# Performance work log

Measured on AMD Instinct MI355X. Metric: run time of the kernel, lower is better.

## Reference

```python
import jax, jax.numpy as jnp
import numpy as np

BN_EPS = 1e-5

def setup_inputs() -> dict:
    key = jax.random.key(0)
    ks = jax.random.split(key, 13)
    bs, ch, hei, wei = 4, 32, 32, 128  # n_features = wei = 128, ch = n_features//4
    nf = wei
    def p(k, shape, s=0.05):
        return jax.random.normal(k, shape, dtype=jnp.float32) * s
    return {
        "head": jax.random.normal(ks[0], (bs, ch, hei, wei), dtype=jnp.float32),
        "tail": jax.random.normal(ks[1], (bs, ch, hei, wei), dtype=jnp.float32),
        "R_q": p(ks[2], (nf, nf)), "R_k": p(ks[3], (nf, nf)),
        "R_v": p(ks[4], (nf, nf)), "R_W": p(ks[5], (nf, nf)),
        "F_q": p(ks[6], (nf, nf)), "F_k": p(ks[7], (nf, nf)),
        "F_v": p(ks[8], (nf, nf)), "F_W": p(ks[9], (nf, nf)),
        "conv_w": p(ks[10], (2, 2 * ch, 1, 1)),
        "conv_b": jnp.zeros((2,), jnp.float32),
        "bn_w": jnp.ones((2,), jnp.float32),
        "bn_b": jnp.zeros((2,), jnp.float32),
        "bn_mean": jnp.zeros((2,), jnp.float32),
        "bn_var": jnp.ones((2,), jnp.float32),
        "flag": 1,
    }

def _affinity(head, tail, conv_w, conv_b, bn_w, bn_b, bn_mean, bn_var):
    # 1x1 conv -> eval-mode BatchNorm2d -> ReLU -> softmax over channel dim
    x = jnp.concatenate([head, tail], axis=1)                       # [b,2c,h,w]
    a = jnp.einsum('bchw,oc->bohw', x, conv_w[:, :, 0, 0]) + conv_b[None, :, None, None]
    scale = (bn_w / jnp.sqrt(bn_var + BN_EPS))[None, :, None, None]
    a = (a - bn_mean[None, :, None, None]) * scale + bn_b[None, :, None, None]
    a = jax.nn.relu(a)
    return jax.nn.softmax(a, axis=1)                                # torch legacy dim=1 for 4D

def reference(head, tail, R_q, R_k, R_v, R_W, F_q, F_k, F_v, F_W,
              conv_w, conv_b, bn_w, bn_b, bn_mean, bn_var, flag):
    bs, ch, hei, wei = head.shape
    L = hei * wei
    ic = ch  # inter_channels == ch by construction
    aff = _affinity(head, tail, conv_w, conv_b, bn_w, bn_b, bn_mean, bn_var)
    if flag:
        alpha = aff[:, 0].reshape(bs, L, 1)                          # broadcast over last axis
        q = (head @ R_q).reshape(bs, ic, L).transpose(0, 2, 1)       # [b,L,ic]
        t_k = (tail @ F_k).reshape(bs, ic, L).transpose(0, 2, 1)     # [b,L,ic]
        t_v = (tail @ F_v).reshape(bs, ic, L)                        # [b,ic,L]
        f_t = t_k @ t_v                                              # [b,L,L]
        h_k = (head @ R_k).reshape(bs, ic, L).transpose(0, 2, 1)
        h_v = (head @ R_v).reshape(bs, ic, L)
        f_h = h_k @ h_v                                              # [b,L,L]
        att = jax.nn.softmax(alpha * f_t + f_h, axis=-1)
        y = (att @ q).transpose(0, 2, 1).reshape(bs, ic, hei, wei)
        return y @ R_W + head
    else:
        alpha = aff[:, 1].reshape(bs, L, 1)
        q = (tail @ F_q).reshape(bs, ic, L).transpose(0, 2, 1)
        h_k = (head @ R_k).reshape(bs, ic, L).transpose(0, 2, 1)
        h_v = (head @ R_v).reshape(bs, ic, L)
        f_h = h_k @ h_v
        t_k = (tail @ F_k).reshape(bs, ic, L).transpose(0, 2, 1)
        t_v = (tail @ F_v).reshape(bs, ic, L)
        f_t = t_k @ t_v
        att = jax.nn.softmax(alpha * f_h + f_t, axis=-1)
        y = (att @ q).transpose(0, 2, 1).reshape(bs, ic, hei, wei)
        return y @ F_W + tail
```

## Files before the change

### kernel.cpp

```cpp
#include <hip/hip_runtime.h>
#include <hip/hip_bf16.h>
#include <stdint.h>

typedef unsigned short u16;
typedef unsigned int u32;
typedef __attribute__((ext_vector_type(8))) short short8;
typedef __attribute__((ext_vector_type(4))) short short4_t;
typedef __attribute__((ext_vector_type(4))) float f32x4;

#define MFMA16(A,B,C) __builtin_amdgcn_mfma_f32_16x16x32_bf16((A),(B),(C),0,0,0)
#define L2E 1.4426950408889634f

__device__ __forceinline__ u16 f2bf(float f) {
  u32 x = __float_as_uint(f);
  u32 r = x + 0x7fffu + ((x >> 16) & 1u);
  return (u16)(r >> 16);
}
__device__ __forceinline__ float bf2f(short v) {
  return __uint_as_float((u32)(u16)v << 16);
}
__device__ __forceinline__ u32 pack_bf2(float a, float b) {
  __hip_bfloat162 h = __float22bfloat162_rn(make_float2(a, b));
  u32 u; __builtin_memcpy(&u, &h, 4); return u;
}
__device__ __forceinline__ short8 mk_frag(u32 w0, u32 w1, u32 w2, u32 w3) {
  union { u32 u[4]; short8 s; } cv;
  cv.u[0] = w0; cv.u[1] = w1; cv.u[2] = w2; cv.u[3] = w3;
  return cv.s;
}

__global__ void kprep(const float* R_q, const float* R_k, const float* R_v,
                      const float* R_W, const float* F_q, const float* F_k,
                      const float* F_v, const float* F_W, const int* flagp,
                      u16* matT)
{
  int flag = *flagp;
  const float* S;
  int m = blockIdx.x;
  if (flag) {
    const float* s[6] = {R_q, R_k, R_v, F_k, F_v, R_W}; S = s[m];
  } else {
    const float* s[6] = {F_q, F_k, F_v, R_k, R_v, F_W}; S = s[m];
  }
  u16* dst = matT + m * 16384;
  int base = blockIdx.y * 2048;
  for (int idx = base + threadIdx.x; idx < base + 2048; idx += blockDim.x) {
    int k = idx >> 7, n = idx & 127;
    dst[n * 128 + k] = f2bf(S[idx]);
  }
}

__global__ __launch_bounds__(256) void kproj(const float* __restrict__ head,
    const float* __restrict__ tail, const u16* __restrict__ matT,
    const float* __restrict__ conv_w, const float* __restrict__ conv_b,
    const float* __restrict__ bn_w, const float* __restrict__ bn_b,
    const float* __restrict__ bn_mean, const float* __restrict__ bn_var,
    u16* __restrict__ qT, u16* __restrict__ KQ,
    u16* __restrict__ Vc, const int* __restrict__ flagp)
{
  __shared__ u16 lds_t[128][34];
  __shared__ float s_alpha[128];
  const int flag = *flagp;
  const float* X1 = flag ? head : tail;
  const float* X2 = flag ? tail : head;
  const int bh = blockIdx.x, g = blockIdx.y;
  const int b = bh >> 5, h = bh & 31;
  const float* src = (g < 3) ? X1 : X2;
  const u16* Bm = matT + g * 16384;
  const int tid = threadIdx.x, lane = tid & 63, wid = tid >> 6;
  const int lrow = lane & 15, lg = lane >> 4;
  const int rt = wid & 1, cbase = (wid >> 1) * 64;

  if (g == 3) {
    if (tid < 128) {
      int w = tid;
      const float* hp = head + ((size_t)b * 1024 + h) * 128 + w;
      const float* tp = tail + ((size_t)b * 1024 + h) * 128 + w;
      float a0 = 0.f, a1 = 0.f;
      for (int c = 0; c < 32; ++c) {
        float xh = hp[c * 4096];
        float xt = tp[c * 4096];
        a0 += xh * conv_w[c]      + xt * conv_w[32 + c];
        a1 += xh * conv_w[64 + c] + xt * conv_w[96 + c];
      }
      const float eps = 1e-5f;
      a0 += conv_b[0]; a1 += conv_b[1];
      a0 = (a0 - bn_mean[0]) * (bn_w[0] * rsqrtf(bn_var[0] + eps)) + bn_b[0];
      a1 = (a1 - bn_mean[1]) * (bn_w[1] * rsqrtf(bn_var[1] + eps)) + bn_b[1];
      a0 = fmaxf(a0, 0.f); a1 = fmaxf(a1, 0.f);
      float asel = flag ? a0 : a1, aoth = flag ? a1 : a0;
      s_alpha[w] = 1.f / (1.f + __expf(aoth - asel));
    }
    __syncthreads();
  }

  f32x4 acc[4] = {};
  const float* Arow = src + (((size_t)b * 32 + rt * 16 + lrow) * 32 + h) * 128;
  #pragma unroll
  for (int k0 = 0; k0 < 128; k0 += 32) {
    short8 af;
    const float* ap = Arow + k0 + lg * 8;
    #pragma unroll
    for (int j = 0; j < 8; ++j) af[j] = (short)f2bf(ap[j]);
    #pragma unroll
    for (int cc = 0; cc < 4; ++cc) {
      short8 bf = *reinterpret_cast<const short8*>(
          Bm + (cbase + cc * 16 + lrow) * 128 + k0 + lg * 8);
      acc[cc] = MFMA16(af, bf, acc[cc]);
    }
  }
  #pragma unroll
  for (int cc = 0; cc < 4; ++cc) {
    int n = cbase + cc * 16 + lrow;
    float asc = (g == 1) ? L2E : 1.f;
    if (g == 3) asc = s_alpha[n] * L2E;
    #pragma unroll
    for (int rr = 0; rr < 4; ++rr) {
      int c = rt * 16 + lg * 4 + rr;
      lds_t[n][c] = f2bf(acc[cc][rr] * asc);
    }
  }
  __syncthreads();
  if (g == 0) {
    int c = tid >> 3, w0 = (tid & 7) * 16;
    int tw[8];
    #pragma unroll
    for (int i2 = 0; i2 < 8; ++i2)
      tw[i2] = (int)lds_t[w0 + 2 * i2][c] | ((int)lds_t[w0 + 2 * i2 + 1][c] << 16);
    int4* dst = reinterpret_cast<int4*>(qT + ((size_t)b * 32 + c) * 4096 + h * 128 + w0);
    dst[0] = make_int4(tw[0], tw[1], tw[2], tw[3]);
    dst[1] = make_int4(tw[4], tw[5], tw[6], tw[7]);
  } else if (tid < 128) {
    int w = tid;
    int tw[16];
    #pragma unroll
    for (int i2 = 0; i2 < 16; ++i2)
      tw[i2] = (int)lds_t[w][2 * i2] | ((int)lds_t[w][2 * i2 + 1] << 16);
    u16* base = (g == 2 || g == 4) ? Vc : KQ;
    int coff = (g >= 3) ? 32 : 0;
    int4* dst = reinterpret_cast<int4*>(base + ((size_t)b * 4096 + h * 128 + w) * 64 + coff);
    dst[0] = make_int4(tw[0],  tw[1],  tw[2],  tw[3]);
    dst[1] = make_int4(tw[4],  tw[5],  tw[6],  tw[7]);
    dst[2] = make_int4(tw[8],  tw[9],  tw[10], tw[11]);
    dst[3] = make_int4(tw[12], tw[13], tw[14], tw[15]);
  }
}

__global__ __launch_bounds__(256, 6) void kattn(const u16* __restrict__ qT,
    const u16* __restrict__ KQ, const u16* __restrict__ Vc,
    u16* __restrict__ pO, float* __restrict__ pm, float* __restrict__ pl)
{
  __shared__ __align__(16) char lds_v[2][8192];
  __shared__ __align__(16) char lds_q[2][4096];
  const int b = blockIdx.y;
  const int i0 = blockIdx.x * 64;
  const int sp = blockIdx.z;
  const int jbase = sp * 512;
  const int tid = threadIdx.x, lane = tid & 63, wid = tid >> 6;
  const int lrow = lane & 15, lg = lane >> 4;

  const u16* KQb = KQ + (size_t)b * 4096 * 64;
  const u16* Vb  = Vc + (size_t)b * 4096 * 64;
  const u16* qTb = qT + (size_t)b * 32 * 4096;

  short8 bkq[2];
  {
    int r = i0 + wid * 16 + lrow;
    #pragma unroll
    for (int kc = 0; kc < 2; ++kc)
      bkq[kc] = *reinterpret_cast<const short8*>(KQb + (size_t)r * 64 + kc * 32 + lg * 8);
  }

  const int sr = tid >> 3, sx = (tid & 7) * 16;
  const int pr = (((sr >> 2) & 3) << 3) + (((sr >> 4) & 1) << 2) + (sr & 3);

  #pragma unroll
  for (int q = 0; q < 2; ++q) {
    int r = sr + q * 32, gr = pr + q * 32;
    int4 v = *reinterpret_cast<const int4*>(
        reinterpret_cast<const char*>(Vb + (size_t)(jbase + gr) * 64) + sx);
    *reinterpret_cast<int4*>(lds_v[0] + r * 128 + (sx ^ ((r & 7) << 4))) = v;
  }
  {
    int4 qv = *reinterpret_cast<const int4*>(
        qTb + (size_t)sr * 4096 + jbase + (tid & 7) * 8);
    *reinterpret_cast<int4*>(lds_q[0] + sr * 128 + (sx ^ ((sr & 7) << 4))) = qv;
  }
  __syncthreads();

  float m_run = -1e30f, l_run = 0.f;
  f32x4 accO[2] = {};
  int4 stgV[2], stgQ;

  for (int t = 0; t < 8; ++t) {
    const int buf = t & 1;
    if (t < 7) {
      const u16* Vn = Vb + (size_t)(jbase + (t + 1) * 64) * 64;
      #pragma unroll
      for (int q = 0; q < 2; ++q) {
        int gr = pr + q * 32;
        stgV[q] = *reinterpret_cast<const int4*>(
            reinterpret_cast<const char*>(Vn + (size_t)gr * 64) + sx);
      }
      stgQ = *reinterpret_cast<const int4*>(
          qTb + (size_t)sr * 4096 + jbase + (t + 1) * 64 + (tid & 7) * 8);
    }
    f32x4 st[4];
    __builtin_amdgcn_s_setprio(1);
    #pragma unroll
    for (int sub = 0; sub < 4; ++sub) {
      f32x4 a = {};
      #pragma unroll
      for (int kc = 0; kc < 2; ++kc) {
        int r = sub * 16 + lrow;
        int xs = kc * 64 + lg * 16;
        short8 av = *reinterpret_cast<const short8*>(
            lds_v[buf] + r * 128 + (xs ^ ((r & 7) << 4)));
        a = MFMA16(av, bkq[kc], a);
      }
      st[sub] = a;
    }
    __builtin_amdgcn_s_setprio(0);
    short8 aq[2][2];
    #pragma unroll
    for (int w = 0; w < 2; ++w)
      #pragma unroll
      for (int ct = 0; ct < 2; ++ct) {
        int r = ct * 16 + lrow;
        int xs = w * 64 + lg * 16;
        aq[w][ct] = *reinterpret_cast<const short8*>(
            lds_q[buf] + r * 128 + (xs ^ ((r & 7) << 4)));
      }
    float tm = -1e30f;
    #pragma unroll
    for (int sub = 0; sub < 4; ++sub)
      #pragma unroll
      for (int rr = 0; rr < 4; ++rr) tm = fmaxf(tm, st[sub][rr]);
    tm = fmaxf(tm, __shfl_xor(tm, 16, 64));
    tm = fmaxf(tm, __shfl_xor(tm, 32, 64));
    if (!__all((int)(tm <= m_run + 8.f))) {
      float m_new = fmaxf(m_run, tm);
      float scale = exp2f(m_run - m_new);
      l_run *= scale;
      #pragma unroll
      for (int ct = 0; ct < 2; ++ct)
        #pragma unroll
        for (int rr = 0; rr < 4; ++rr) accO[ct][rr] *= scale;
      m_run = m_new;
    }
    float ps = 0.f;
    #pragma unroll
    for (int sub = 0; sub < 4; ++sub)
      #pragma unroll
      for (int rr = 0; rr < 4; ++rr) {
        float p = exp2f(st[sub][rr] - m_run);
        st[sub][rr] = p;
        ps += p;
      }
    ps += __shfl_xor(ps, 16, 64);
    ps += __shfl_xor(ps, 32, 64);
    l_run += ps;

    __builtin_amdgcn_s_setprio(1);
    #pragma unroll
    for (int w = 0; w < 2; ++w) {
      short8 bp = mk_frag(pack_bf2(st[2 * w][0],     st[2 * w][1]),
                          pack_bf2(st[2 * w][2],     st[2 * w][3]),
                          pack_bf2(st[2 * w + 1][0], st[2 * w + 1][1]),
                          pack_bf2(st[2 * w + 1][2], st[2 * w + 1][3]));
      #pragma unroll
      for (int ct = 0; ct < 2; ++ct)
        accO[ct] = MFMA16(aq[w][ct], bp, accO[ct]);
    }
    __builtin_amdgcn_s_setprio(0);

    if (t < 7) {
      #pragma unroll
      for (int q = 0; q < 2; ++q) {
        int r = sr + q * 32;
        *reinterpret_cast<int4*>(lds_v[buf ^ 1] + r * 128 + (sx ^ ((r & 7) << 4))) = stgV[q];
      }
      *reinterpret_cast<int4*>(lds_q[buf ^ 1] + sr * 128 + (sx ^ ((sr & 7) << 4))) = stgQ;
      __syncthreads();
    }
  }

  const int i = i0 + wid * 16 + lrow;
  u16* pOb = pO + (size_t)((b * 8 + sp) * 32) * 4096;
  #pragma unroll
  for (int ct = 0; ct < 2; ++ct)
    #pragma unroll
    for (int rr = 0; rr < 4; ++rr)
      pOb[(size_t)(ct * 16 + lg * 4 + rr) * 4096 + i] = f2bf(accO[ct][rr]);
  if (lg == 0) {
    pm[(b * 8 + sp) * 4096 + i] = m_run;
    pl[(b * 8 + sp) * 4096 + i] = l_run;
  }
}

__global__ __launch_bounds__(128) void kout(const u16* __restrict__ pO,
    const float* __restrict__ pm, const float* __restrict__ pl,
    const u16* __restrict__ matT, const float* __restrict__ head,
    const float* __restrict__ tail, const int* __restrict__ flagp,
    float* __restrict__ out)
{
  __shared__ u16 ylds[16][136];
  const int flag = *flagp;
  const float* X1 = flag ? head : tail;
  const u16* Bm = matT + 5 * 16384;
  const int tid = threadIdx.x;
  const int rbase = blockIdx.x * 16;
  const int b = rbase >> 10, c = (rbase >> 5) & 31, h0 = rbase & 31;
  const int ioff = h0 * 128 + tid * 16;

  #pragma unroll
  for (int iq = 0; iq < 4; ++iq) {
    float4 msp[8];
    #pragma unroll
    for (int sp = 0; sp < 8; ++sp)
      msp[sp] = *reinterpret_cast<const float4*>(
          pm + (size_t)((b * 8 + sp) * 4096) + ioff + iq * 4);
    float4 M4 = msp[0];
    #pragma unroll
    for (int sp = 1; sp < 8; ++sp) {
      M4.x = fmaxf(M4.x, msp[sp].x); M4.y = fmaxf(M4.y, msp[sp].y);
      M4.z = fmaxf(M4.z, msp[sp].z); M4.w = fmaxf(M4.w, msp[sp].w);
    }
    float4 L4 = {0.f, 0.f, 0.f, 0.f}, y4 = {0.f, 0.f, 0.f, 0.f};
    #pragma unroll
    for (int sp = 0; sp < 8; ++sp) {
      float4 w4;
      w4.x = exp2f(msp[sp].x - M4.x); w4.y = exp2f(msp[sp].y - M4.y);
      w4.z = exp2f(msp[sp].z - M4.z); w4.w = exp2f(msp[sp].w - M4.w);
      float4 l4 = *reinterpret_cast<const float4*>(
          pl + (size_t)((b * 8 + sp) * 4096) + ioff + iq * 4);
      L4.x += w4.x * l4.x; L4.y += w4.y * l4.y;
      L4.z += w4.z * l4.z; L4.w += w4.w * l4.w;
      short4_t o4 = *reinterpret_cast<const short4_t*>(
          pO + (size_t)(((b * 8 + sp) * 32 + c)) * 4096 + ioff + iq * 4);
      y4.x += w4.x * bf2f(o4[0]); y4.y += w4.y * bf2f(o4[1]);
      y4.z += w4.z * bf2f(o4[2]); y4.w += w4.w * bf2f(o4[3]);
    }
    y4.x /= L4.x; y4.y /= L4.y; y4.z /= L4.z; y4.w /= L4.w;
    uint2 pk2;
    pk2.x = pack_bf2(y4.x, y4.y);
    pk2.y = pack_bf2(y4.z, y4.w);
    *reinterpret_cast<uint2*>(&ylds[tid >> 3][(tid & 7) * 16 + iq * 4]) = pk2;
  }
  __syncthreads();

  const int lane = tid & 63, wid = tid >> 6;
  const int lrow = lane & 15, lg = lane >> 4;
  const int ctbase = wid * 4;
  f32x4 acc[4] = {};
  #pragma unroll
  for (int k0 = 0; k0 < 128; k0 += 32) {
    short8 af = *reinterpret_cast<const short8*>(&ylds[lrow][k0 + lg * 8]);
    #pragma unroll
    for (int cc = 0; cc < 4; ++cc) {
      short8 bf = *reinterpret_cast<const short8*>(
          Bm + (size_t)((ctbase + cc) * 16 + lrow) * 128 + k0 + lg * 8);
      acc[cc] = MFMA16(af, bf, acc[cc]);
    }
  }
  #pragma unroll
  for (int cc = 0; cc < 4; ++cc)
    #pragma unroll
    for (int rr = 0; rr < 4; ++rr) {
      int row = rbase + lg * 4 + rr;
      int col = (ctbase + cc) * 16 + lrow;
      size_t idx = (size_t)row * 128 + col;
      out[idx] = acc[cc][rr] + X1[idx];
    }
}

extern "C" void kernel_launch(void* const* d_in, const int* in_sizes, int n_in,
                              void* d_out, int out_size, void* d_ws, size_t ws_size,
                              hipStream_t stream)
{
  const float* head    = (const float*)d_in[0];
  const float* tail    = (const float*)d_in[1];
  const float* R_q     = (const float*)d_in[2];
  const float* R_k     = (const float*)d_in[3];
  const float* R_v     = (const float*)d_in[4];
  const float* R_W     = (const float*)d_in[5];
  const float* F_q     = (const float*)d_in[6];
  const float* F_k     = (const float*)d_in[7];
  const float* F_v     = (const float*)d_in[8];
  const float* F_W     = (const float*)d_in[9];
  const float* conv_w  = (const float*)d_in[10];
  const float* conv_b  = (const float*)d_in[11];
  const float* bn_w    = (const float*)d_in[12];
  const float* bn_b    = (const float*)d_in[13];
  const float* bn_mean = (const float*)d_in[14];
  const float* bn_var  = (const float*)d_in[15];
  const int*   flagp   = (const int*)d_in[16];
  float* out = (float*)d_out;

  char* ws = (char*)d_ws;
  u16*   matT = (u16*)(ws);
  u16*   qT   = (u16*)(ws + 262144);
  u16*   KQ   = (u16*)(ws + 1310720);
  u16*   Vc   = (u16*)(ws + 3407872);
  u16*   pO   = (u16*)(ws + 6553600);
  float* pm   = (float*)(ws + 14942208);
  float* pl   = (float*)(ws + 15466496);

  kprep <<<dim3(6, 8), 256, 0, stream>>>(R_q, R_k, R_v, R_W, F_q, F_k, F_v, F_W, flagp, matT);
  kproj <<<dim3(128, 5), 256, 0, stream>>>(head, tail, matT, conv_w, conv_b,
                                           bn_w, bn_b, bn_mean, bn_var,
                                           qT, KQ, Vc, flagp);
  kattn <<<dim3(64, 4, 8), 256, 0, stream>>>(qT, KQ, Vc, pO, pm, pl);
  kout  <<<256, 128, 0, stream>>>(pO, pm, pl, matT, head, tail, flagp, out);
}
```

Measured before the change: 63.08 us.

## Process two 64-row query tiles per attention block to reuse staged K/V tiles

Each attention block now covers 128 query rows instead of 64. Every wave holds two independent online-softmax states and reuses each LDS-staged V and q tile for both row groups. This halves the global-to-LDS staging traffic and the number of blocks (grid 1024 instead of 2048). In exchange it raises register pressure, with launch bounds relaxed from 6 to 4 waves, and reduces the parallelism available to hide latency.

```diff
diff --git a/kernel.cpp b/kernel.cpp
--- a/kernel.cpp
+++ b/kernel.cpp
@@ -27,6 +27,12 @@
   union { u32 u[4]; short8 s; } cv;
   cv.u[0] = w0; cv.u[1] = w1; cv.u[2] = w2; cv.u[3] = w3;
   return cv.s;
+}
+__device__ __forceinline__ float vmax4(f32x4 v) {
+  return fmaxf(fmaxf(v[0], v[1]), fmaxf(v[2], v[3]));
+}
+__device__ __forceinline__ float vsum4(f32x4 v) {
+  return (v[0] + v[1]) + (v[2] + v[3]);
 }
 
 __global__ void kprep(const float* R_q, const float* R_k, const float* R_v,
@@ -146,14 +152,14 @@
   }
 }
 
-__global__ __launch_bounds__(256, 6) void kattn(const u16* __restrict__ qT,
+__global__ __launch_bounds__(256, 4) void kattn(const u16* __restrict__ qT,
     const u16* __restrict__ KQ, const u16* __restrict__ Vc,
     u16* __restrict__ pO, float* __restrict__ pm, float* __restrict__ pl)
 {
   __shared__ __align__(16) char lds_v[2][8192];
   __shared__ __align__(16) char lds_q[2][4096];
   const int b = blockIdx.y;
-  const int i0 = blockIdx.x * 64;
+  const int i0 = blockIdx.x * 128;
   const int sp = blockIdx.z;
   const int jbase = sp * 512;
   const int tid = threadIdx.x, lane = tid & 63, wid = tid >> 6;
@@ -163,12 +169,13 @@
   const u16* Vb  = Vc + (size_t)b * 4096 * 64;
   const u16* qTb = qT + (size_t)b * 32 * 4096;
 
-  short8 bkq[2];
-  {
-    int r = i0 + wid * 16 + lrow;
+  short8 bkq[2][2];
+  #pragma unroll
+  for (int it = 0; it < 2; ++it) {
+    int r = i0 + it * 64 + wid * 16 + lrow;
     #pragma unroll
     for (int kc = 0; kc < 2; ++kc)
-      bkq[kc] = *reinterpret_cast<const short8*>(KQb + (size_t)r * 64 + kc * 32 + lg * 8);
+      bkq[it][kc] = *reinterpret_cast<const short8*>(KQb + (size_t)r * 64 + kc * 32 + lg * 8);
   }
 
   const int sr = tid >> 3, sx = (tid & 7) * 16;
@@ -188,8 +195,8 @@
   }
   __syncthreads();
 
-  float m_run = -1e30f, l_run = 0.f;
-  f32x4 accO[2] = {};
+  float m_run[2] = {-1e30f, -1e30f}, l_run[2] = {0.f, 0.f};
+  f32x4 accO[2][2] = {};
   int4 stgV[2], stgQ;
 
   for (int t = 0; t < 8; ++t) {
@@ -205,20 +212,25 @@
       stgQ = *reinterpret_cast<const int4*>(
           qTb + (size_t)sr * 4096 + jbase + (t + 1) * 64 + (tid & 7) * 8);
     }
-    f32x4 st[4];
+    f32x4 st[2][4];
     __builtin_amdgcn_s_setprio(1);
     #pragma unroll
     for (int sub = 0; sub < 4; ++sub) {
-      f32x4 a = {};
+      short8 av[2];
       #pragma unroll
       for (int kc = 0; kc < 2; ++kc) {
         int r = sub * 16 + lrow;
         int xs = kc * 64 + lg * 16;
-        short8 av = *reinterpret_cast<const short8*>(
+        av[kc] = *reinterpret_cast<const short8*>(
             lds_v[buf] + r * 128 + (xs ^ ((r & 7) << 4)));
-        a = MFMA16(av, bkq[kc], a);
-      }
-      st[sub] = a;
+      }
+      #pragma unroll
+      for (int it = 0; it < 2; ++it) {
+        f32x4 a = {};
+        a = MFMA16(av[0], bkq[it][0], a);
+        a = MFMA16(av[1], bkq[it][1], a);
+        st[it][sub] = a;
+      }
     }
     __builtin_amdgcn_s_setprio(0);
     short8 aq[2][2];
@@ -231,47 +243,47 @@
         aq[w][ct] = *reinterpret_cast<const short8*>(
             lds_q[buf] + r * 128 + (xs ^ ((r & 7) << 4)));
       }
-    float tm = -1e30f;
-    #pragma unroll
-    for (int sub = 0; sub < 4; ++sub)
-      #pragma unroll
-      for (int rr = 0; rr < 4; ++rr) tm = fmaxf(tm, st[sub][rr]);
-    tm = fmaxf(tm, __shfl_xor(tm, 16, 64));
-    tm = fmaxf(tm, __shfl_xor(tm, 32, 64));
-    if (!__all((int)(tm <= m_run + 8.f))) {
-      float m_new = fmaxf(m_run, tm);
-      float scale = exp2f(m_run - m_new);
-      l_run *= scale;
-      #pragma unroll
-      for (int ct = 0; ct < 2; ++ct)
+    #pragma unroll
+    for (int it = 0; it < 2; ++it) {
+      float tm = fmaxf(fmaxf(vmax4(st[it][0]), vmax4(st[it][1])),
+                       fmaxf(vmax4(st[it][2]), vmax4(st[it][3])));
+      tm = fmaxf(tm, __shfl_xor(tm, 16, 64));
+      tm = fmaxf(tm, __shfl_xor(tm, 32, 64));
+      if (!__all((int)(tm <= m_run[it] + 8.f))) {
+        float m_new = fmaxf(m_run[it], tm);
+        float scale = exp2f(m_run[it] - m_new);
+        l_run[it] *= scale;
         #pragma unroll
-        for (int rr = 0; rr < 4; ++rr) accO[ct][rr] *= scale;
-      m_run = m_new;
-    }
-    float ps = 0.f;
-    #pragma unroll
-    for (int sub = 0; sub < 4; ++sub)
-      #pragma unroll
-      for (int rr = 0; rr < 4; ++rr) {
-        float p = exp2f(st[sub][rr] - m_run);
-        st[sub][rr] = p;
-        ps += p;
-      }
-    ps += __shfl_xor(ps, 16, 64);
-    ps += __shfl_xor(ps, 32, 64);
-    l_run += ps;
+        for (int ct = 0; ct < 2; ++ct)
+          #pragma unroll
+          for (int rr = 0; rr < 4; ++rr) accO[it][ct][rr] *= scale;
+        m_run[it] = m_new;
+      }
+      #pragma unroll
+      for (int sub = 0; sub < 4; ++sub)
+        #pragma unroll
+        for (int rr = 0; rr < 4; ++rr)
+          st[it][sub][rr] = exp2f(st[it][sub][rr] - m_run[it]);
+      float ps = (vsum4(st[it][0]) + vsum4(st[it][1])) +
+                 (vsum4(st[it][2]) + vsum4(st[it][3]));
+      ps += __shfl_xor(ps, 16, 64);
+      ps += __shfl_xor(ps, 32, 64);
+      l_run[it] += ps;
+    }
 
     __builtin_amdgcn_s_setprio(1);
     #pragma unroll
-    for (int w = 0; w < 2; ++w) {
-      short8 bp = mk_frag(pack_bf2(st[2 * w][0],     st[2 * w][1]),
-                          pack_bf2(st[2 * w][2],     st[2 * w][3]),
-                          pack_bf2(st[2 * w + 1][0], st[2 * w + 1][1]),
-                          pack_bf2(st[2 * w + 1][2], st[2 * w + 1][3]));
-      #pragma unroll
-      for (int ct = 0; ct < 2; ++ct)
-        accO[ct] = MFMA16(aq[w][ct], bp, accO[ct]);
-    }
+    for (int it = 0; it < 2; ++it)
+      #pragma unroll
+      for (int w = 0; w < 2; ++w) {
+        short8 bp = mk_frag(pack_bf2(st[it][2 * w][0],     st[it][2 * w][1]),
+                            pack_bf2(st[it][2 * w][2],     st[it][2 * w][3]),
+                            pack_bf2(st[it][2 * w + 1][0], st[it][2 * w + 1][1]),
+                            pack_bf2(st[it][2 * w + 1][2], st[it][2 * w + 1][3]));
+        #pragma unroll
+        for (int ct = 0; ct < 2; ++ct)
+          accO[it][ct] = MFMA16(aq[w][ct], bp, accO[it][ct]);
+      }
     __builtin_amdgcn_s_setprio(0);
 
     if (t < 7) {
@@ -285,16 +297,19 @@
     }
   }
 
-  const int i = i0 + wid * 16 + lrow;
   u16* pOb = pO + (size_t)((b * 8 + sp) * 32) * 4096;
   #pragma unroll
-  for (int ct = 0; ct < 2; ++ct)
-    #pragma unroll
-    for (int rr = 0; rr < 4; ++rr)
-      pOb[(size_t)(ct * 16 + lg * 4 + rr) * 4096 + i] = f2bf(accO[ct][rr]);
-  if (lg == 0) {
-    pm[(b * 8 + sp) * 4096 + i] = m_run;
-    pl[(b * 8 + sp) * 4096 + i] = l_run;
+  for (int it = 0; it < 2; ++it) {
+    const int i = i0 + it * 64 + wid * 16 + lrow;
+    #pragma unroll
+    for (int ct = 0; ct < 2; ++ct)
+      #pragma unroll
+      for (int rr = 0; rr < 4; ++rr)
+        pOb[(size_t)(ct * 16 + lg * 4 + rr) * 4096 + i] = f2bf(accO[it][ct][rr]);
+    if (lg == 0) {
+      pm[(b * 8 + sp) * 4096 + i] = m_run[it];
+      pl[(b * 8 + sp) * 4096 + i] = l_run[it];
+    }
   }
 }
 
@@ -410,6 +425,6 @@
   kproj <<<dim3(128, 5), 256, 0, stream>>>(head, tail, matT, conv_w, conv_b,
                                            bn_w, bn_b, bn_mean, bn_var,
                                            qT, KQ, Vc, flagp);
-  kattn <<<dim3(64, 4, 8), 256, 0, stream>>>(qT, KQ, Vc, pO, pm, pl);
+  kattn <<<dim3(32, 4, 8), 256, 0, stream>>>(qT, KQ, Vc, pO, pm, pl);
   kout  <<<256, 128, 0, stream>>>(pO, pm, pl, matT, head, tail, flagp, out);
 }
```

Result: slower. 64.65 us (+2.5%).
